# Performance work log

Hardware: AMD Instinct MI355X
Metric: run time of the kernel (lower is better)

## Reference

```python
import jax, jax.numpy as jnp
import numpy as np

NUM_NODES = 50000
NUM_EDGES = 800000
NUM_FEATURES = 128
HIDDEN = 256
NUM_CLASSES = 10
NUM_GRAPHS = 64


def setup_inputs() -> dict:
    key = jax.random.key(0)
    ks = jax.random.split(key, 16)
    x = jax.random.normal(ks[0], (NUM_NODES, NUM_FEATURES), dtype=jnp.float32)
    edge_index = jax.random.randint(ks[1], (2, NUM_EDGES), 0, NUM_NODES, dtype=jnp.int64)
    batch = jnp.sort(jax.random.randint(ks[2], (NUM_NODES,), 0, NUM_GRAPHS, dtype=jnp.int64))

    def glorot(k, shape):
        fan_in, fan_out = shape[-2], shape[-1]
        s = jnp.sqrt(6.0 / (fan_in + fan_out)).astype(jnp.float32)
        return jax.random.uniform(k, shape, jnp.float32, -s, s)

    inp = {
        "x": x, "edge_index": edge_index, "batch": batch,
        # Chebyshev weights: one [in, out] matrix per hop order k
        "W1": glorot(ks[3], (3, NUM_FEATURES, HIDDEN)), "b1": jnp.zeros((HIDDEN,), jnp.float32),
        "W2": glorot(ks[4], (4, HIDDEN, HIDDEN)),       "b2": jnp.zeros((HIDDEN,), jnp.float32),
        "W3": glorot(ks[5], (5, HIDDEN, HIDDEN)),       "b3": jnp.zeros((HIDDEN,), jnp.float32),
        "fc1_w": glorot(ks[6], (HIDDEN, 512)),  "fc1_b": jnp.zeros((512,), jnp.float32),
        "fc2_w": glorot(ks[7], (512, HIDDEN)),  "fc2_b": jnp.zeros((HIDDEN,), jnp.float32),
        "fc3_w": glorot(ks[8], (HIDDEN, NUM_CLASSES)), "fc3_b": jnp.zeros((NUM_CLASSES,), jnp.float32),
    }
    return inp


def reference(x, edge_index, batch, W1, b1, W2, b2, W3, b3,
              fc1_w, fc1_b, fc2_w, fc2_b, fc3_w, fc3_b):
    N = x.shape[0]
    src, dst = edge_index[0], edge_index[1]

    # Scaled Laplacian L_hat = -D^{-1/2} A D^{-1/2} (lambda_max = 2, sym norm)
    deg = jax.ops.segment_sum(jnp.ones_like(src, dtype=x.dtype), src, num_segments=N)
    dis = jnp.where(deg > 0, jax.lax.rsqrt(jnp.maximum(deg, 1.0)), 0.0)
    w = -dis[src] * dis[dst]  # [E]

    def prop(h):  # L_hat @ h via gather-scale-scatter
        return jax.ops.segment_sum(h[src] * w[:, None], dst, num_segments=N)

    def cheb(h, Wk, b):
        K = Wk.shape[0]
        Tx0 = h
        out = Tx0 @ Wk[0]
        Tx1 = prop(h)
        out = out + Tx1 @ Wk[1]
        for k in range(2, K):
            Tx2 = 2.0 * prop(Tx1) - Tx0
            out = out + Tx2 @ Wk[k]
            Tx0, Tx1 = Tx1, Tx2
        return out + b

    h = jax.nn.relu(cheb(x, W1, b1))
    h = jax.nn.relu(cheb(h, W2, b2))
    h = jax.nn.relu(cheb(h, W3, b3))

    # global mean pool over graphs in the batch
    sums = jax.ops.segment_sum(h, batch, num_segments=NUM_GRAPHS)
    cnts = jax.ops.segment_sum(jnp.ones((N,), h.dtype), batch, num_segments=NUM_GRAPHS)
    g = sums / jnp.maximum(cnts, 1.0)[:, None]  # [G, 256]

    g = jax.nn.relu(g @ fc1_w + fc1_b)  # dropout is identity at inference
    g = jax.nn.relu(g @ fc2_w + fc2_b)
    g = g @ fc3_w + fc3_b
    return jax.nn.log_softmax(g, axis=1)
```

## Files before the change

### kernel.cpp

```cpp
#include <hip/hip_runtime.h>
#include <cstdint>
#include <cstddef>

#define NN 50000
#define NE 800000
#define FIN 128
#define HID 256
#define NCLS 10
#define NG 64
#define LDT 1280

#define NCH 13
#define NCELL (NN * NCH)
#define NSCB ((NCELL + 255) / 256)

typedef unsigned int uint;
typedef unsigned short ushort;
typedef __attribute__((ext_vector_type(8))) short short8;
typedef __attribute__((ext_vector_type(4))) float f32x4;

static inline size_t align_up(size_t v, size_t a) { return (v + a - 1) / a * a; }

__device__ __forceinline__ float bf2f(ushort u) {
    union { uint i; float f; } v; v.i = (uint)u << 16; return v.f;
}
__device__ __forceinline__ ushort f2bf(float f) {
    union { uint i; float f; } v; v.f = f;
    uint i = v.i;
    uint r = (i + 0x7fffu + ((i >> 16) & 1u)) >> 16;
    return (ushort)r;
}
__device__ __forceinline__ uint pack2(float a, float b) {
    return (uint)f2bf(a) | ((uint)f2bf(b) << 16);
}


__global__ void k_degcnt(const int* __restrict__ src, const int* __restrict__ dst,
                         int* __restrict__ ideg, int* __restrict__ cellcnt) {
    int e = blockIdx.x * 256 + threadIdx.x;
    if (e < NE) {
        int s = src[e], d = dst[e];
        atomicAdd(&ideg[s], 1);
        atomicAdd(&cellcnt[d * NCH + (s >> 12)], 1);
    }
}

__global__ void k_dis(const int* __restrict__ ideg, float* __restrict__ dis) {
    int n = blockIdx.x * 256 + threadIdx.x;
    if (n < NN) {
        int d = ideg[n];
        dis[n] = (d > 0) ? rsqrtf((float)d) : 0.0f;
    }
}

__global__ void k_scanA(const int* __restrict__ cnt, int* __restrict__ rp,
                        int* __restrict__ bsum) {
    __shared__ int s[256];
    int i = blockIdx.x * 256 + threadIdx.x;
    int v = (i < NCELL) ? cnt[i] : 0;
    s[threadIdx.x] = v;
    __syncthreads();
    for (int off = 1; off < 256; off <<= 1) {
        int t = (threadIdx.x >= (unsigned)off) ? s[threadIdx.x - off] : 0;
        __syncthreads();
        s[threadIdx.x] += t;
        __syncthreads();
    }
    if (i < NCELL) rp[i] = s[threadIdx.x] - v;
    if (threadIdx.x == 255) bsum[blockIdx.x] = s[255];
}

__global__ void k_scanB(int* __restrict__ b, int n) {
    __shared__ int s[1024];
    __shared__ int carry;
    if (threadIdx.x == 0) carry = 0;
    __syncthreads();
    for (int base = 0; base < n; base += 1024) {
        int i = base + threadIdx.x;
        int v = (i < n) ? b[i] : 0;
        s[threadIdx.x] = v;
        __syncthreads();
        for (int off = 1; off < 1024; off <<= 1) {
            int t = (threadIdx.x >= (unsigned)off) ? s[threadIdx.x - off] : 0;
            __syncthreads();
            s[threadIdx.x] += t;
            __syncthreads();
        }
        int c = carry;
        if (i < n) b[i] = c + s[threadIdx.x] - v;
        __syncthreads();
        if (threadIdx.x == 0) carry = c + s[1023];
        __syncthreads();
    }
}

__global__ void k_scanC(const int* __restrict__ bsum, int* __restrict__ rp,
                        int* __restrict__ cur, int* __restrict__ rpn) {
    int i = blockIdx.x * 256 + threadIdx.x;
    if (i < NCELL) {
        int v = rp[i] + bsum[blockIdx.x];
        rp[i] = v;
        cur[i] = v;
        if (i % NCH == 0) rpn[i / NCH] = v;
    }
    if (i == 0) rpn[NN] = NE;
}

__global__ void k_fill2(const int* __restrict__ src, const int* __restrict__ dst,
                        const float* __restrict__ dis, int* __restrict__ cur,
                        uint2* __restrict__ em) {
    int e = blockIdx.x * 256 + threadIdx.x;
    if (e < NE) {
        int s = src[e], d = dst[e];
        int pos = atomicAdd(&cur[d * NCH + (s >> 12)], 1);
        uint2 m;
        m.x = (uint)s;
        m.y = __float_as_uint(-dis[s] * dis[d]);
        em[pos] = m;
    }
}

__global__ void k_wt(const float* __restrict__ W, ushort* __restrict__ Wt, int K) {
    int i = blockIdx.x * 256 + threadIdx.x;
    if (i < K * 256) {
        int k = i >> 8, n = i & 255;
        Wt[(size_t)n * K + k] = f2bf(W[i]);
    }
}


__global__ void k_spread_x(const float* __restrict__ x, ushort* __restrict__ T) {
    int i = blockIdx.x * 256 + threadIdx.x;
    if (i < NN * 64) {
        int m = i >> 6, p = i & 63;
        const float* xp = x + (size_t)m * FIN + p * 2;
        uint* tp = (uint*)(T + (size_t)m * LDT) + p;
        *tp = pack2(xp[0], xp[1]);
    }
}

template <int FUSE, int F>
__global__ __launch_bounds__(512) void k_prop3(
    const int* __restrict__ rpn, const uint2* __restrict__ em,
    const ushort* __restrict__ h, const ushort* __restrict__ sub,
    ushort* __restrict__ out) {
    constexpr int NV = (F == 256) ? 4 : 2;
    int d = blockIdx.x * 8 + (threadIdx.x >> 6);
    int lane = threadIdx.x & 63;
    int beg = rpn[d], end = rpn[d + 1];
    float a[NV];
#pragma unroll
    for (int j = 0; j < NV; ++j) a[j] = 0.0f;

    int e = beg;
    for (; e + 8 <= end; e += 8) {
        uint2 mt[8];
#pragma unroll
        for (int u = 0; u < 8; ++u) mt[u] = em[e + u];
        if (F == 256) {
            uint2 gg[8];
#pragma unroll
            for (int u = 0; u < 8; ++u)
                gg[u] = *((const uint2*)(h + (size_t)mt[u].x * LDT) + lane);
#pragma unroll
            for (int u = 0; u < 8; ++u) {
                float wv = __uint_as_float(mt[u].y);
                a[0] += wv * bf2f((ushort)gg[u].x);
                a[1] += wv * bf2f((ushort)(gg[u].x >> 16));
                a[2] += wv * bf2f((ushort)gg[u].y);
                a[3] += wv * bf2f((ushort)(gg[u].y >> 16));
            }
        } else {
            uint gg[8];
#pragma unroll
            for (int u = 0; u < 8; ++u)
                gg[u] = *((const uint*)(h + (size_t)mt[u].x * LDT) + lane);
#pragma unroll
            for (int u = 0; u < 8; ++u) {
                float wv = __uint_as_float(mt[u].y);
                a[0] += wv * bf2f((ushort)gg[u]);
                a[1] += wv * bf2f((ushort)(gg[u] >> 16));
            }
        }
    }
    for (; e + 4 <= end; e += 4) {
        uint2 mt[4];
#pragma unroll
        for (int u = 0; u < 4; ++u) mt[u] = em[e + u];
        if (F == 256) {
            uint2 gg[4];
#pragma unroll
            for (int u = 0; u < 4; ++u)
                gg[u] = *((const uint2*)(h + (size_t)mt[u].x * LDT) + lane);
#pragma unroll
            for (int u = 0; u < 4; ++u) {
                float wv = __uint_as_float(mt[u].y);
                a[0] += wv * bf2f((ushort)gg[u].x);
                a[1] += wv * bf2f((ushort)(gg[u].x >> 16));
                a[2] += wv * bf2f((ushort)gg[u].y);
                a[3] += wv * bf2f((ushort)(gg[u].y >> 16));
            }
        } else {
            uint gg[4];
#pragma unroll
            for (int u = 0; u < 4; ++u)
                gg[u] = *((const uint*)(h + (size_t)mt[u].x * LDT) + lane);
#pragma unroll
            for (int u = 0; u < 4; ++u) {
                float wv = __uint_as_float(mt[u].y);
                a[0] += wv * bf2f((ushort)gg[u]);
                a[1] += wv * bf2f((ushort)(gg[u] >> 16));
            }
        }
    }
    for (; e < end; ++e) {
        uint2 m0 = em[e];
        float w0 = __uint_as_float(m0.y);
        if (F == 256) {
            uint2 g0 = *((const uint2*)(h + (size_t)m0.x * LDT) + lane);
            a[0] += w0 * bf2f((ushort)g0.x); a[1] += w0 * bf2f((ushort)(g0.x >> 16));
            a[2] += w0 * bf2f((ushort)g0.y); a[3] += w0 * bf2f((ushort)(g0.y >> 16));
        } else {
            uint g0 = *((const uint*)(h + (size_t)m0.x * LDT) + lane);
            a[0] += w0 * bf2f((ushort)g0); a[1] += w0 * bf2f((ushort)(g0 >> 16));
        }
    }

    if (F == 256) {
        uint2* op = (uint2*)(out + (size_t)d * LDT) + lane;
        if (FUSE) {
            uint2 sv = *((const uint2*)(sub + (size_t)d * LDT) + lane);
            uint2 r;
            r.x = pack2(2.0f * a[0] - bf2f((ushort)sv.x),
                        2.0f * a[1] - bf2f((ushort)(sv.x >> 16)));
            r.y = pack2(2.0f * a[2] - bf2f((ushort)sv.y),
                        2.0f * a[3] - bf2f((ushort)(sv.y >> 16)));
            *op = r;
        } else {
            uint2 r;
            r.x = pack2(a[0], a[1]);
            r.y = pack2(a[2], a[3]);
            *op = r;
        }
    } else {
        uint* op = (uint*)(out + (size_t)d * LDT) + lane;
        if (FUSE) {
            uint sv = *((const uint*)(sub + (size_t)d * LDT) + lane);
            *op = pack2(2.0f * a[0] - bf2f((ushort)sv),
                        2.0f * a[1] - bf2f((ushort)(sv >> 16)));
        } else {
            *op = pack2(a[0], a[1]);
        }
    }
}

template <int K>
__global__ __launch_bounds__(256) void k_mm2(
    const ushort* __restrict__ A, int lda,
    int m0, int m1, int m2, int m3, int m4,
    const ushort* __restrict__ Wt, const float* __restrict__ bias,
    ushort* __restrict__ H, int ldh, int M) {
    constexpr int NT = K / 32;
    __shared__ ushort As[2][128 * 32];
    __shared__ ushort Bs[2][128 * 32];
    int tid = threadIdx.x;
    int lane = tid & 63, w = tid >> 6;
    int wm = w >> 1, wn = w & 1;
    int rowBase = blockIdx.x * 128;
    int colBase = blockIdx.y * 128;
    int srow = lane >> 2;
    int c16 = lane & 3;

    f32x4 acc[4][4];
#pragma unroll
    for (int i = 0; i < 4; ++i)
#pragma unroll
        for (int j = 0; j < 4; ++j) acc[i][j] = (f32x4){0.f, 0.f, 0.f, 0.f};

    auto stage = [&](int t) {
        int kk = t * 32;
        int slot = kk >> 8;
        int coff = (slot == 0 ? m0 : slot == 1 ? m1 : slot == 2 ? m2
                    : slot == 3 ? m3 : m4) + (kk & 255);
        int b = t & 1;
#pragma unroll
        for (int q = 0; q < 2; ++q) {
            int seg = w * 2 + q;
            int r = seg * 16 + srow;
            int cs = c16 ^ ((r >> 1) & 3);
            int grow = rowBase + r;
            if (grow > M - 1) grow = M - 1;
            const ushort* gp = A + (size_t)grow * lda + coff + cs * 8;
            __builtin_amdgcn_global_load_lds(
                (const __attribute__((address_space(1))) void*)gp,
                (__attribute__((address_space(3))) void*)((char*)&As[b][0] + seg * 1024),
                16, 0, 0);
        }
#pragma unroll
        for (int q = 0; q < 2; ++q) {
            int seg = w * 2 + q;
            int r = seg * 16 + srow;
            int cs = c16 ^ ((r >> 1) & 3);
            const ushort* gp = Wt + (size_t)(colBase + r) * K + kk + cs * 8;
            __builtin_amdgcn_global_load_lds(
                (const __attribute__((address_space(1))) void*)gp,
                (__attribute__((address_space(3))) void*)((char*)&Bs[b][0] + seg * 1024),
                16, 0, 0);
        }
    };

    stage(0);
    asm volatile("s_waitcnt vmcnt(0)" ::: "memory");
    __builtin_amdgcn_s_barrier();

    for (int t = 0; t < NT; ++t) {
        if (t + 1 < NT) stage(t + 1);
        int b = t & 1;
        short8 af[4], bf[4];
#pragma unroll
        for (int mi = 0; mi < 4; ++mi) {
            int r = wm * 64 + mi * 16 + (lane & 15);
            int j = (lane >> 4) ^ ((r >> 1) & 3);
            af[mi] = *(const short8*)((const char*)&As[b][0] + r * 64 + j * 16);
        }
#pragma unroll
        for (int ni = 0; ni < 4; ++ni) {
            int r = wn * 64 + ni * 16 + (lane & 15);
            int j = (lane >> 4) ^ ((r >> 1) & 3);
            bf[ni] = *(const short8*)((const char*)&Bs[b][0] + r * 64 + j * 16);
        }
#pragma unroll
        for (int mi = 0; mi < 4; ++mi)
#pragma unroll
            for (int ni = 0; ni < 4; ++ni)
                acc[mi][ni] = __builtin_amdgcn_mfma_f32_16x16x32_bf16(
                    af[mi], bf[ni], acc[mi][ni], 0, 0, 0);
        asm volatile("s_waitcnt vmcnt(0)" ::: "memory");
        __builtin_amdgcn_s_barrier();
    }

    int lg = lane >> 4;
    float bv[4];
#pragma unroll
    for (int ni = 0; ni < 4; ++ni)
        bv[ni] = bias[colBase + wn * 64 + ni * 16 + (lane & 15)];
#pragma unroll
    for (int mi = 0; mi < 4; ++mi) {
#pragma unroll
        for (int r = 0; r < 4; ++r) {
            int row = rowBase + wm * 64 + mi * 16 + lg * 4 + r;
            if (row >= M) continue;
#pragma unroll
            for (int ni = 0; ni < 4; ++ni) {
                int colL = colBase + wn * 64 + ni * 16 + (lane & 15);
                float v = acc[mi][ni][r] + bv[ni];
                v = fmaxf(v, 0.0f);
                H[(size_t)row * ldh + colL] = f2bf(v);
            }
        }
    }
}


__global__ void k_pool(const ushort* __restrict__ h, const int* __restrict__ batch,
                       float* __restrict__ sums, float* __restrict__ cnts) {
    int f = threadIdx.x;
    int n0 = blockIdx.x * 128;
    if (n0 >= NN) return;
    int nEnd = n0 + 128 < NN ? n0 + 128 : NN;
    int cur = batch[n0];
    float acc = 0.0f, c = 0.0f;
    for (int n = n0; n < nEnd; ++n) {
        int b = batch[n];
        if (b != cur) {
            atomicAdd(&sums[cur * HID + f], acc);
            if (f == 0) atomicAdd(&cnts[cur], c);
            acc = 0.0f; c = 0.0f; cur = b;
        }
        acc += bf2f(h[(size_t)n * HID + f]);
        c += 1.0f;
    }
    atomicAdd(&sums[cur * HID + f], acc);
    if (f == 0) atomicAdd(&cnts[cur], c);
}

__global__ void k_gdiv(const float* __restrict__ sums, const float* __restrict__ cnts,
                       float* __restrict__ g) {
    int i = blockIdx.x * 256 + threadIdx.x;
    int b = i >> 8;
    g[i] = sums[i] / fmaxf(cnts[b], 1.0f);
}


template <int RELU>
__global__ void k_fc(const float* __restrict__ in, const float* __restrict__ W,
                     const float* __restrict__ bias, float* __restrict__ out,
                     int K, int Nc) {
    __shared__ float s[512];
    int gi = blockIdx.x;
    for (int i = threadIdx.x; i < K; i += blockDim.x) s[i] = in[gi * K + i];
    __syncthreads();
    int c = blockIdx.y * blockDim.x + threadIdx.x;
    if (c < Nc) {
        float acc = bias[c];
        for (int k = 0; k < K; ++k) acc += s[k] * W[k * Nc + c];
        out[gi * Nc + c] = RELU ? fmaxf(acc, 0.0f) : acc;
    }
}

__global__ void k_fc3_lsm(const float* __restrict__ in, const float* __restrict__ W,
                          const float* __restrict__ b, float* __restrict__ out) {
    __shared__ float s[HID];
    __shared__ float lg[NCLS];
    int gi = blockIdx.x;
    s[threadIdx.x] = in[gi * HID + threadIdx.x];
    __syncthreads();
    if (threadIdx.x < NCLS) {
        float acc = b[threadIdx.x];
        for (int k = 0; k < HID; ++k) acc += s[k] * W[k * NCLS + threadIdx.x];
        lg[threadIdx.x] = acc;
    }
    __syncthreads();
    if (threadIdx.x < NCLS) {
        float m = -1e30f;
        for (int c = 0; c < NCLS; ++c) m = fmaxf(m, lg[c]);
        float sum = 0.0f;
        for (int c = 0; c < NCLS; ++c) sum += expf(lg[c] - m);
        out[gi * NCLS + threadIdx.x] = lg[threadIdx.x] - m - logf(sum);
    }
}


extern "C" void kernel_launch(void* const* d_in, const int* in_sizes, int n_in,
                              void* d_out, int out_size, void* d_ws, size_t ws_size,
                              hipStream_t stream) {
    const float* x = (const float*)d_in[0];
    const int* ei = (const int*)d_in[1];
    const int* src = ei;
    const int* dst = ei + NE;
    const int* batch = (const int*)d_in[2];
    const float* W1 = (const float*)d_in[3];
    const float* b1 = (const float*)d_in[4];
    const float* W2 = (const float*)d_in[5];
    const float* b2 = (const float*)d_in[6];
    const float* W3 = (const float*)d_in[7];
    const float* b3 = (const float*)d_in[8];
    const float* fc1w = (const float*)d_in[9];
    const float* fc1b = (const float*)d_in[10];
    const float* fc2w = (const float*)d_in[11];
    const float* fc2b = (const float*)d_in[12];
    const float* fc3w = (const float*)d_in[13];
    const float* fc3b = (const float*)d_in[14];
    float* out = (float*)d_out;

    char* p = (char*)d_ws;
    auto carve = [&](size_t bytes) {
        char* r = p;
        p += align_up(bytes, 256);
        return (void*)r;
    };
    ushort* Tbig = (ushort*)carve((size_t)NN * LDT * 2);
    ushort* hA = (ushort*)carve((size_t)NN * HID * 2);
    ushort* Wt1 = (ushort*)carve((size_t)HID * 384 * 2);
    ushort* Wt2 = (ushort*)carve((size_t)HID * 1024 * 2);
    ushort* Wt3 = (ushort*)carve((size_t)HID * 1280 * 2);
    int* ideg = (int*)carve((size_t)NN * 4);
    float* dis = (float*)carve((size_t)NN * 4);
    uint2* em = (uint2*)carve((size_t)NE * 8);
    int* cellcnt = (int*)carve((size_t)NCELL * 4);
    int* cellptr = (int*)carve((size_t)(NCELL + 1) * 4);
    int* ccur = (int*)carve((size_t)NCELL * 4);
    int* rpn = (int*)carve((size_t)(NN + 1) * 4);
    int* bsum = (int*)carve((size_t)NSCB * 4);
    float* psum = (float*)carve((size_t)NG * HID * 4);
    float* pcnt = (float*)carve((size_t)NG * 4);
    float* g = (float*)carve((size_t)NG * HID * 4);
    float* f1 = (float*)carve((size_t)NG * 512 * 4);
    float* f2 = (float*)carve((size_t)NG * HID * 4);

    hipMemsetAsync(ideg, 0, (size_t)NN * 4, stream);
    hipMemsetAsync(cellcnt, 0, (size_t)NCELL * 4, stream);
    hipMemsetAsync(psum, 0, (size_t)NG * HID * 4, stream);
    hipMemsetAsync(pcnt, 0, (size_t)NG * 4, stream);

    k_degcnt<<<(NE + 255) / 256, 256, 0, stream>>>(src, dst, ideg, cellcnt);
    k_dis<<<(NN + 255) / 256, 256, 0, stream>>>(ideg, dis);
    k_scanA<<<NSCB, 256, 0, stream>>>(cellcnt, cellptr, bsum);
    k_scanB<<<1, 1024, 0, stream>>>(bsum, NSCB);
    k_scanC<<<NSCB, 256, 0, stream>>>(bsum, cellptr, ccur, rpn);
    k_fill2<<<(NE + 255) / 256, 256, 0, stream>>>(src, dst, dis, ccur, em);

    k_wt<<<(384 * 256 + 255) / 256, 256, 0, stream>>>(W1, Wt1, 384);
    k_wt<<<(1024 * 256 + 255) / 256, 256, 0, stream>>>(W2, Wt2, 1024);
    k_wt<<<(1280 * 256 + 255) / 256, 256, 0, stream>>>(W3, Wt3, 1280);

    dim3 mmg((NN + 127) / 128, 2);

    k_spread_x<<<(NN * 64 + 255) / 256, 256, 0, stream>>>(x, Tbig);
    k_prop3<0, 128><<<NN / 8, 512, 0, stream>>>(rpn, em, Tbig + 0, nullptr, Tbig + 128);
    k_prop3<1, 128><<<NN / 8, 512, 0, stream>>>(rpn, em, Tbig + 128, Tbig + 0, Tbig + 256);
    k_mm2<384><<<mmg, 256, 0, stream>>>(Tbig, LDT, 0, 256, 0, 0, 0,
                                        Wt1, b1, Tbig + 1024, LDT, NN);

    k_prop3<0, 256><<<NN / 8, 512, 0, stream>>>(rpn, em, Tbig + 1024, nullptr, Tbig + 0);
    k_prop3<1, 256><<<NN / 8, 512, 0, stream>>>(rpn, em, Tbig + 0, Tbig + 1024, Tbig + 256);
    k_prop3<1, 256><<<NN / 8, 512, 0, stream>>>(rpn, em, Tbig + 256, Tbig + 0, Tbig + 512);
    k_mm2<1024><<<mmg, 256, 0, stream>>>(Tbig, LDT, 1024, 0, 256, 512, 0,
                                         Wt2, b2, Tbig + 768, LDT, NN);

    k_prop3<0, 256><<<NN / 8, 512, 0, stream>>>(rpn, em, Tbig + 768, nullptr, Tbig + 1024);
    k_prop3<1, 256><<<NN / 8, 512, 0, stream>>>(rpn, em, Tbig + 1024, Tbig + 768, Tbig + 0);
    k_prop3<1, 256><<<NN / 8, 512, 0, stream>>>(rpn, em, Tbig + 0, Tbig + 1024, Tbig + 256);
    k_prop3<1, 256><<<NN / 8, 512, 0, stream>>>(rpn, em, Tbig + 256, Tbig + 0, Tbig + 512);
    k_mm2<1280><<<mmg, 256, 0, stream>>>(Tbig, LDT, 768, 1024, 0, 256, 512,
                                         Wt3, b3, hA, HID, NN);

    k_pool<<<(NN + 127) / 128, 256, 0, stream>>>(hA, batch, psum, pcnt);
    k_gdiv<<<(NG * HID) / 256, 256, 0, stream>>>(psum, pcnt, g);
    k_fc<1><<<dim3(NG, 2), 256, 0, stream>>>(g, fc1w, fc1b, f1, HID, 512);
    k_fc<1><<<dim3(NG, 1), 256, 0, stream>>>(f1, fc2w, fc2b, f2, 512, HID);
    k_fc3_lsm<<<NG, 256, 0, stream>>>(f2, fc3w, fc3b, out);
}
```

Measured before the change: 880.9 us.

## Triple-buffer GEMM LDS staging and prefetch edge metadata in prop gather loop

The GEMM kernel moves from double to triple-buffered LDS staging. It keeps two stages in flight with a partial vmcnt wait and a single barrier per k-step, so global loads overlap MFMA work further. The propagation kernel software-pipelines the edge-metadata loads, fetching the next 8 edges' indices and weights while the current gathers are in flight. This costs more LDS (lower occupancy risk) and more registers in prop, and the vmcnt(4) count must match the number of loads issued per stage.

```diff
diff --git a/kernel.cpp b/kernel.cpp
--- a/kernel.cpp
+++ b/kernel.cpp
@@ -153,34 +153,51 @@
     for (int j = 0; j < NV; ++j) a[j] = 0.0f;
 
     int e = beg;
-    for (; e + 8 <= end; e += 8) {
+    int nfull = (end - beg) >> 3;
+    if (nfull > 0) {
         uint2 mt[8];
 #pragma unroll
         for (int u = 0; u < 8; ++u) mt[u] = em[e + u];
-        if (F == 256) {
-            uint2 gg[8];
-#pragma unroll
-            for (int u = 0; u < 8; ++u)
-                gg[u] = *((const uint2*)(h + (size_t)mt[u].x * LDT) + lane);
-#pragma unroll
-            for (int u = 0; u < 8; ++u) {
-                float wv = __uint_as_float(mt[u].y);
-                a[0] += wv * bf2f((ushort)gg[u].x);
-                a[1] += wv * bf2f((ushort)(gg[u].x >> 16));
-                a[2] += wv * bf2f((ushort)gg[u].y);
-                a[3] += wv * bf2f((ushort)(gg[u].y >> 16));
+        for (int g = 0; g < nfull; ++g) {
+            uint2 mtn[8];
+            if (F == 256) {
+                uint2 gg[8];
+#pragma unroll
+                for (int u = 0; u < 8; ++u)
+                    gg[u] = *((const uint2*)(h + (size_t)mt[u].x * LDT) + lane);
+#pragma unroll
+                for (int u = 0; u < 8; ++u) {
+                    int pe = e + 8 + u; if (pe > end - 1) pe = end - 1;
+                    mtn[u] = em[pe];
+                }
+#pragma unroll
+                for (int u = 0; u < 8; ++u) {
+                    float wv = __uint_as_float(mt[u].y);
+                    a[0] += wv * bf2f((ushort)gg[u].x);
+                    a[1] += wv * bf2f((ushort)(gg[u].x >> 16));
+                    a[2] += wv * bf2f((ushort)gg[u].y);
+                    a[3] += wv * bf2f((ushort)(gg[u].y >> 16));
+                }
+            } else {
+                uint gg[8];
+#pragma unroll
+                for (int u = 0; u < 8; ++u)
+                    gg[u] = *((const uint*)(h + (size_t)mt[u].x * LDT) + lane);
+#pragma unroll
+                for (int u = 0; u < 8; ++u) {
+                    int pe = e + 8 + u; if (pe > end - 1) pe = end - 1;
+                    mtn[u] = em[pe];
+                }
+#pragma unroll
+                for (int u = 0; u < 8; ++u) {
+                    float wv = __uint_as_float(mt[u].y);
+                    a[0] += wv * bf2f((ushort)gg[u]);
+                    a[1] += wv * bf2f((ushort)(gg[u] >> 16));
+                }
             }
-        } else {
-            uint gg[8];
-#pragma unroll
-            for (int u = 0; u < 8; ++u)
-                gg[u] = *((const uint*)(h + (size_t)mt[u].x * LDT) + lane);
-#pragma unroll
-            for (int u = 0; u < 8; ++u) {
-                float wv = __uint_as_float(mt[u].y);
-                a[0] += wv * bf2f((ushort)gg[u]);
-                a[1] += wv * bf2f((ushort)(gg[u] >> 16));
-            }
+#pragma unroll
+            for (int u = 0; u < 8; ++u) mt[u] = mtn[u];
+            e += 8;
         }
     }
     for (; e + 4 <= end; e += 4) {
@@ -255,14 +272,14 @@
 }
 
 template <int K>
-__global__ __launch_bounds__(256) void k_mm2(
+__global__ __launch_bounds__(256) void k_mm3(
     const ushort* __restrict__ A, int lda,
     int m0, int m1, int m2, int m3, int m4,
     const ushort* __restrict__ Wt, const float* __restrict__ bias,
     ushort* __restrict__ H, int ldh, int M) {
     constexpr int NT = K / 32;
-    __shared__ ushort As[2][128 * 32];
-    __shared__ ushort Bs[2][128 * 32];
+    __shared__ ushort As[3][128 * 32];
+    __shared__ ushort Bs[3][128 * 32];
     int tid = threadIdx.x;
     int lane = tid & 63, w = tid >> 6;
     int wm = w >> 1, wn = w & 1;
@@ -282,7 +299,7 @@
         int slot = kk >> 8;
         int coff = (slot == 0 ? m0 : slot == 1 ? m1 : slot == 2 ? m2
                     : slot == 3 ? m3 : m4) + (kk & 255);
-        int b = t & 1;
+        int b = t % 3;
 #pragma unroll
         for (int q = 0; q < 2; ++q) {
             int seg = w * 2 + q;
@@ -310,12 +327,18 @@
     };
 
     stage(0);
-    asm volatile("s_waitcnt vmcnt(0)" ::: "memory");
-    __builtin_amdgcn_s_barrier();
+    stage(1);
 
     for (int t = 0; t < NT; ++t) {
-        if (t + 1 < NT) stage(t + 1);
-        int b = t & 1;
+        if (t + 1 < NT) {
+            asm volatile("s_waitcnt vmcnt(4)" ::: "memory");
+        } else {
+            asm volatile("s_waitcnt vmcnt(0)" ::: "memory");
+        }
+        __builtin_amdgcn_s_barrier();
+        if (t + 2 < NT) stage(t + 2);
+
+        int b = t % 3;
         short8 af[4], bf[4];
 #pragma unroll
         for (int mi = 0; mi < 4; ++mi) {
@@ -335,8 +358,6 @@
             for (int ni = 0; ni < 4; ++ni)
                 acc[mi][ni] = __builtin_amdgcn_mfma_f32_16x16x32_bf16(
                     af[mi], bf[ni], acc[mi][ni], 0, 0, 0);
-        asm volatile("s_waitcnt vmcnt(0)" ::: "memory");
-        __builtin_amdgcn_s_barrier();
     }
 
     int lg = lane >> 4;
@@ -499,20 +520,20 @@
     k_spread_x<<<(NN * 64 + 255) / 256, 256, 0, stream>>>(x, Tbig);
     k_prop3<0, 128><<<NN / 8, 512, 0, stream>>>(rpn, em, Tbig + 0, nullptr, Tbig + 128);
     k_prop3<1, 128><<<NN / 8, 512, 0, stream>>>(rpn, em, Tbig + 128, Tbig + 0, Tbig + 256);
-    k_mm2<384><<<mmg, 256, 0, stream>>>(Tbig, LDT, 0, 256, 0, 0, 0,
+    k_mm3<384><<<mmg, 256, 0, stream>>>(Tbig, LDT, 0, 256, 0, 0, 0,
                                         Wt1, b1, Tbig + 1024, LDT, NN);
 
     k_prop3<0, 256><<<NN / 8, 512, 0, stream>>>(rpn, em, Tbig + 1024, nullptr, Tbig + 0);
     k_prop3<1, 256><<<NN / 8, 512, 0, stream>>>(rpn, em, Tbig + 0, Tbig + 1024, Tbig + 256);
     k_prop3<1, 256><<<NN / 8, 512, 0, stream>>>(rpn, em, Tbig + 256, Tbig + 0, Tbig + 512);
-    k_mm2<1024><<<mmg, 256, 0, stream>>>(Tbig, LDT, 1024, 0, 256, 512, 0,
+    k_mm3<1024><<<mmg, 256, 0, stream>>>(Tbig, LDT, 1024, 0, 256, 512, 0,
                                          Wt2, b2, Tbig + 768, LDT, NN);
 
     k_prop3<0, 256><<<NN / 8, 512, 0, stream>>>(rpn, em, Tbig + 768, nullptr, Tbig + 1024);
     k_prop3<1, 256><<<NN / 8, 512, 0, stream>>>(rpn, em, Tbig + 1024, Tbig + 768, Tbig + 0);
     k_prop3<1, 256><<<NN / 8, 512, 0, stream>>>(rpn, em, Tbig + 0, Tbig + 1024, Tbig + 256);
     k_prop3<1, 256><<<NN / 8, 512, 0, stream>>>(rpn, em, Tbig + 256, Tbig + 0, Tbig + 512);
-    k_mm2<1280><<<mmg, 256, 0, stream>>>(Tbig, LDT, 768, 1024, 0, 256, 512,
+    k_mm3<1280><<<mmg, 256, 0, stream>>>(Tbig, LDT, 768, 1024, 0, 256, 512,
                                          Wt3, b3, hA, HID, NN);
 
     k_pool<<<(NN + 127) / 128, 256, 0, stream>>>(hA, batch, psum, pcnt);
```

New measurement: 932.0 us. +5.8%, slower.
